# Kernel tuning notes

Measured on AMD Instinct MI355X. Metric: run time of the kernel, lower is better.

## Reference

```python
import jax, jax.numpy as jnp
import numpy as np

OUT = 3      # pooled output size (fmap_size//4 = 14//4 = 3)
RATIO = 2    # roi_align sampling ratio (fixed; torchvision adaptive ratio for 14/3 bins is 2)
P = 20       # num_persons


def _bilinear(fm, y, x):
    # fm: [C,H,W]; y,x broadcastable coordinate grids. torchvision aligned=False semantics.
    C, H, W = fm.shape
    y, x = jnp.broadcast_arrays(y, x)
    valid = (y > -1.0) & (y < H) & (x > -1.0) & (x < W)
    y = jnp.clip(y, 0.0, H - 1.0)
    x = jnp.clip(x, 0.0, W - 1.0)
    y0 = jnp.floor(y).astype(jnp.int32)
    x0 = jnp.floor(x).astype(jnp.int32)
    y1 = jnp.minimum(y0 + 1, H - 1)
    x1 = jnp.minimum(x0 + 1, W - 1)
    ly = y - y0
    lx = x - x0
    hy = 1.0 - ly
    hx = 1.0 - lx
    v00 = fm[:, y0, x0]
    v01 = fm[:, y0, x1]
    v10 = fm[:, y1, x0]
    v11 = fm[:, y1, x1]
    val = hy * hx * v00 + hy * lx * v01 + ly * hx * v10 + ly * lx * v11
    return jnp.where(valid, val, 0.0)  # [C, ...]


def _roi_align_one(fm, box):
    # fm: [C,H,W], box: [4] = (x1,y1,x2,y2) in feature-map coords -> [C,OUT,OUT]
    x1, y1, x2, y2 = box
    bw = (x2 - x1) / OUT
    bh = (y2 - y1) / OUT
    off = (jnp.arange(OUT * RATIO, dtype=fm.dtype) + 0.5) / RATIO  # bin-unit offsets
    xs = x1 + off * bw
    ys = y1 + off * bh
    vals = _bilinear(fm, ys[:, None], xs[None, :])  # [C, OUT*RATIO, OUT*RATIO]
    C = fm.shape[0]
    return vals.reshape(C, OUT, RATIO, OUT, RATIO).mean(axis=(2, 4))


def setup_inputs() -> dict:
    key = jax.random.key(0)
    ks = jax.random.split(key, 8)
    B, N, NB, C, FS = 128, 8, 27, 1024, 14
    fmap = jax.random.normal(ks[0], (B, C, FS, FS), jnp.float32)
    # boxes in feature-map coordinates with x1<x2, y1<y2
    lo = jax.random.uniform(ks[1], (B, N, 2), jnp.float32) * 10.0
    ext = 2.0 + jax.random.uniform(ks[2], (B, N, 2), jnp.float32) * 4.0
    hi = jnp.minimum(lo + ext, float(FS))
    boxes = jnp.concatenate([lo, hi], axis=-1)  # [B,N,4] (x1,y1,x2,y2)
    # unique person ids per frame (scatter target indices)
    pids = jax.vmap(lambda k: jax.random.permutation(k, P)[:N])(jax.random.split(ks[3], B)).astype(jnp.int32)
    w1 = jax.random.normal(ks[4], (512, C), jnp.float32) * 0.02
    w2 = jax.random.normal(ks[5], (256, 512), jnp.float32) * 0.05
    fc1_w = jax.random.normal(ks[6], (1024, 256 * OUT * OUT), jnp.float32) * 0.02
    fc1_b = jnp.zeros((1024,), jnp.float32)
    fc2_w = jax.random.normal(ks[7], (27, 1024), jnp.float32) * 0.02
    fc2_b = jnp.zeros((27,), jnp.float32)
    return {"fmap": fmap, "boxes": boxes, "pids": pids, "w1": w1, "w2": w2,
            "fc1_w": fc1_w, "fc1_b": fc1_b, "fc2_w": fc2_w, "fc2_b": fc2_b}


def _forward(fmap, boxes, pids, w1, w2, fc1_w, fc1_b, fc2_w, fc2_b):
    B, N = boxes.shape[:2]
    # per-image, per-box ROI align: [B,N,C,3,3]
    roi = jax.vmap(jax.vmap(_roi_align_one, in_axes=(None, 0)), in_axes=(0, 0))(fmap, boxes)
    # behavior_conv: two bias-free 1x1 convs (no nonlinearity between)
    h = jnp.einsum('bnchw,oc->bnohw', roi, w1)
    h = jnp.einsum('bnchw,oc->bnohw', h, w2)  # [B,N,256,3,3]
    feat = h.reshape(B, N, -1)                # [B,N,2304]
    bidx = jnp.broadcast_to(jnp.arange(B)[:, None], (B, N))
    # scatter into behavior_tensor keyed by person id (unique pids per frame -> well-defined)
    bt = jnp.zeros((B, P, feat.shape[-1]), feat.dtype).at[bidx, pids].set(feat)
    mean_b = bt.mean(axis=0)                  # [P,2304] mean over batch
    cur = bt[bidx, pids]                      # [B,N,2304]
    diff = mean_b[pids] - cur
    # behavior_fc (dropout is identity at inference)
    h1 = jax.nn.relu(jnp.einsum('bnd,hd->bnh', diff, fc1_w) + fc1_b)
    return jnp.einsum('bnh,oh->bno', h1, fc2_w) + fc2_b  # [B,N,num_behaviors]


def reference(fmap, boxes, pids, w1, w2, fc1_w, fc1_b, fc2_w, fc2_b):
    # fmap is detached and roi_align runs under no_grad in the original
    return _forward(jax.lax.stop_gradient(fmap), jax.lax.stop_gradient(boxes), pids,
                    w1, w2, fc1_w, fc1_b, fc2_w, fc2_b)
```

## Files before the change

### kernel.cpp

```cpp
#include <hip/hip_runtime.h>
#include <hip/hip_bf16.h>
#include <cstddef>
#include <cstdint>

#define B_   128
#define N_   8
#define C_   1024
#define FS_  14
#define POS_ 196
#define P_   20
#define HWC_ 9
#define CMID_ 256
#define FEATD_ 2304
#define H1_  1024
#define O_   27

typedef __attribute__((ext_vector_type(8))) short bf16x8;
typedef __attribute__((ext_vector_type(4))) float f32x4;

__device__ __forceinline__ void gld16(const void* g, void* l) {
    __builtin_amdgcn_global_load_lds(
        (const __attribute__((address_space(1))) unsigned int*)g,
        (__attribute__((address_space(3))) unsigned int*)l, 16, 0, 0);
}

__global__ __launch_bounds__(256) void wcombine_split_kernel(
    const float* __restrict__ w1,
    const float* __restrict__ w2,
    float* __restrict__ wpart)
{
    const int tid = threadIdx.x;
    const int tx = tid & 15, ty = tid >> 4;
    const int c0 = blockIdx.x * 64;
    const int o0 = blockIdx.y * 64;
    const int kb = blockIdx.z * 64;
    __shared__ __align__(16) float As[16][68];
    __shared__ __align__(16) float Bs[16][68];
    float acc[4][4] = {};
    for (int k0 = kb; k0 < kb + 64; k0 += 16) {
        for (int i = tid; i < 64 * 16; i += 256) {
            int k = i & 15, m = i >> 4;
            As[k][m] = w2[(size_t)(o0 + m) * 512 + k0 + k];
        }
        for (int i = tid; i < 64 * 16; i += 256) {
            int n = i & 63, k = i >> 6;
            Bs[k][n] = w1[(size_t)(k0 + k) * 1024 + c0 + n];
        }
        __syncthreads();
        #pragma unroll
        for (int k = 0; k < 16; ++k) {
            float4 a = *(const float4*)&As[k][ty * 4];
            float4 b = *(const float4*)&Bs[k][tx * 4];
            float av[4] = {a.x, a.y, a.z, a.w};
            float bv[4] = {b.x, b.y, b.z, b.w};
            #pragma unroll
            for (int i = 0; i < 4; ++i)
                #pragma unroll
                for (int j = 0; j < 4; ++j)
                    acc[i][j] += av[i] * bv[j];
        }
        __syncthreads();
    }
    float* dst = wpart + (size_t)blockIdx.z * (256 * 1024);
    for (int i = 0; i < 4; ++i) {
        float4 v = make_float4(acc[i][0], acc[i][1], acc[i][2], acc[i][3]);
        *(float4*)&dst[(size_t)(o0 + ty * 4 + i) * 1024 + c0 + tx * 4] = v;
    }
}

__global__ __launch_bounds__(256) void wc_reduce_kernel(
    const float* __restrict__ wpart, __hip_bfloat16* __restrict__ Wc)
{
    int idx = blockIdx.x * 256 + threadIdx.x;
    float s = 0.f;
    #pragma unroll
    for (int z = 0; z < 8; ++z) s += wpart[(size_t)z * (256 * 1024) + idx];
    Wc[idx] = __float2bfloat16(s);
}

#define SSTR_  232
#define AROWS_ 72
#define BOFF_  (AROWS_ * SSTR_)
#define PSTR_  72
#define POFF_  (BOFF_ + 64 * SSTR_)
struct bf4s { __hip_bfloat162 lo, hi; };
__global__ __launch_bounds__(256, 2) void poolmix_kernel(
    const float* __restrict__ fmap,
    const float* __restrict__ boxes,
    const __hip_bfloat16* __restrict__ Wc,
    float* __restrict__ featp)
{
    const int cq = blockIdx.x;
    const int b  = blockIdx.y;
    const int tid = threadIdx.x;
    const int wave = tid >> 6, lane = tid & 63;
    const int m16 = lane & 15, quad = lane >> 4;
    __shared__ __align__(16) __hip_bfloat16 Ls[POFF_ + AROWS_ * PSTR_];

    if (tid < AROWS_) {
        const int m = tid;
        const int n = m / 9, cell = m - n * 9;
        const int chh = cell / 3, cww = cell % 3;
        float4 bx = *(const float4*)(boxes + ((size_t)b * N_ + n) * 4);
        float bw = (bx.z - bx.x) * (1.0f / 3.0f);
        float bh = (bx.w - bx.y) * (1.0f / 3.0f);
        float ypro[FS_], xpro[FS_];
        #pragma unroll
        for (int k = 0; k < FS_; ++k) { ypro[k] = 0.f; xpro[k] = 0.f; }
        #pragma unroll
        for (int s = 0; s < 2; ++s) {
            float yy = bx.y + ((float)(2 * chh + s) + 0.5f) * 0.5f * bh;
            bool vy = (yy > -1.0f) && (yy < (float)FS_);
            float y = fminf(fmaxf(yy, 0.0f), (float)(FS_ - 1));
            int y0 = (int)floorf(y);
            int y1i = min(y0 + 1, FS_ - 1);
            float ly = y - (float)y0, hy = 1.0f - ly;
            float qy = vy ? 0.5f : 0.0f;
            float w0 = hy * qy, w1 = ly * qy;
            #pragma unroll
            for (int k = 0; k < FS_; ++k)
                ypro[k] += (k == y0 ? w0 : 0.f) + (k == y1i ? w1 : 0.f);
            float xx = bx.x + ((float)(2 * cww + s) + 0.5f) * 0.5f * bw;
            bool vx = (xx > -1.0f) && (xx < (float)FS_);
            float x = fminf(fmaxf(xx, 0.0f), (float)(FS_ - 1));
            int x0 = (int)floorf(x);
            int x1i = min(x0 + 1, FS_ - 1);
            float lx = x - (float)x0, hx = 1.0f - lx;
            float qx = vx ? 0.5f : 0.0f;
            float u0 = hx * qx, u1 = lx * qx;
            #pragma unroll
            for (int k = 0; k < FS_; ++k)
                xpro[k] += (k == x0 ? u0 : 0.f) + (k == x1i ? u1 : 0.f);
        }
        __hip_bfloat162* row2 = (__hip_bfloat162*)&Ls[m * SSTR_];
        #pragma unroll
        for (int p = 0; p < 98; ++p) {
            const int i0 = 2 * p, i1 = 2 * p + 1;
            __hip_bfloat162 t;
            t.x = __float2bfloat16(ypro[i0 / FS_] * xpro[i0 % FS_]);
            t.y = __float2bfloat16(ypro[i1 / FS_] * xpro[i1 % FS_]);
            row2[p] = t;
        }
        const __hip_bfloat16 z16 = __float2bfloat16(0.0f);
        #pragma unroll
        for (int p = 98; p < SSTR_ / 2; ++p) {
            __hip_bfloat162 t; t.x = z16; t.y = z16;
            row2[p] = t;
        }
    }
    for (int i = tid; i < 64 * 18; i += 256) {
        int r = i / 18, kd = i - r * 18;
        *(unsigned int*)&Ls[BOFF_ + r * SSTR_ + 196 + kd * 2] = 0;
    }

    f32x4 acc2[5][4];
    #pragma unroll
    for (int mt = 0; mt < 5; ++mt)
        #pragma unroll
        for (int nt = 0; nt < 4; ++nt)
            acc2[mt][nt] = (f32x4){0.f, 0.f, 0.f, 0.f};

    const int cbase0 = cq * 512;
    for (int c = 0; c < 8; ++c) {
        const float* src = fmap + ((size_t)b * C_ + cbase0 + c * 64) * POS_;
        #pragma unroll
        for (int it = 0; it < 13; ++it) {
            int i = tid + it * 256;
            if (i < 64 * 49) {
                int cr = i / 49, ch = i - cr * 49;
                float4 v = *(const float4*)(src + (size_t)cr * POS_ + ch * 4);
                bf4s t;
                t.lo.x = __float2bfloat16(v.x); t.lo.y = __float2bfloat16(v.y);
                t.hi.x = __float2bfloat16(v.z); t.hi.y = __float2bfloat16(v.w);
                *(bf4s*)&Ls[BOFF_ + cr * SSTR_ + ch * 4] = t;
            }
        }
        __syncthreads();

        f32x4 acc1[5];
        #pragma unroll
        for (int mt = 0; mt < 5; ++mt) acc1[mt] = (f32x4){0.f, 0.f, 0.f, 0.f};
        const int nrow = wave * 16 + m16;
        #pragma unroll
        for (int kk = 0; kk < 7; ++kk) {
            bf16x8 bfv = *(const bf16x8*)&Ls[BOFF_ + nrow * SSTR_ + kk * 32 + quad * 8];
            #pragma unroll
            for (int mt = 0; mt < 5; ++mt) {
                bf16x8 af = *(const bf16x8*)&Ls[(mt * 16 + m16) * SSTR_ + kk * 32 + quad * 8];
                acc1[mt] = __builtin_amdgcn_mfma_f32_16x16x32_bf16(af, bfv, acc1[mt], 0, 0, 0);
            }
        }
        #pragma unroll
        for (int mt = 0; mt < 5; ++mt) {
            #pragma unroll
            for (int g = 0; g < 4; ++g) {
                int cell = mt * 16 + quad * 4 + g;
                if (cell < AROWS_)
                    Ls[POFF_ + cell * PSTR_ + wave * 16 + m16] =
                        __float2bfloat16(acc1[mt][g]);
            }
        }
        __syncthreads();

        #pragma unroll
        for (int ks = 0; ks < 2; ++ks) {
            bf16x8 af[5];
            #pragma unroll
            for (int mt = 0; mt < 5; ++mt)
                af[mt] = *(const bf16x8*)&Ls[POFF_ + (mt * 16 + m16) * PSTR_ + ks * 32 + quad * 8];
            #pragma unroll
            for (int nt = 0; nt < 4; ++nt) {
                int n = wave * 64 + nt * 16 + m16;
                bf16x8 bfv = *(const bf16x8*)(Wc + (size_t)n * C_ + cbase0 + c * 64 + ks * 32 + quad * 8);
                #pragma unroll
                for (int mt = 0; mt < 5; ++mt)
                    acc2[mt][nt] = __builtin_amdgcn_mfma_f32_16x16x32_bf16(
                        af[mt], bfv, acc2[mt][nt], 0, 0, 0);
            }
        }
    }

    float* dst = featp + (size_t)cq * (128 * AROWS_ * 256);
    #pragma unroll
    for (int mt = 0; mt < 5; ++mt) {
        #pragma unroll
        for (int g = 0; g < 4; ++g) {
            int row = mt * 16 + quad * 4 + g;
            if (row < AROWS_) {
                #pragma unroll
                for (int nt = 0; nt < 4; ++nt)
                    dst[(size_t)(b * AROWS_ + row) * 256 + wave * 64 + nt * 16 + m16] =
                        acc2[mt][nt][g];
            }
        }
    }
}

__global__ __launch_bounds__(256, 4) void fc1_gemm_kernel(
    const __hip_bfloat16* __restrict__ A,
    const __hip_bfloat16* __restrict__ Bm,
    const float* __restrict__ bias,
    float* __restrict__ C)
{
    const int tid = threadIdx.x;
    const int wave = tid >> 6, lane = tid & 63;
    const int r0 = blockIdx.y * 32, n0 = blockIdx.x * 64;
    const int wm = (wave >> 1) * 16, wn = (wave & 1) * 32;
    const int m16 = lane & 15, quad = lane >> 4;
    const int K = FEATD_;
    __shared__ __align__(16) __hip_bfloat16 As[32 * 64];
    __shared__ __align__(16) __hip_bfloat16 Bs[64 * 64];

    f32x4 acc[2];
    acc[0] = (f32x4){0.f, 0.f, 0.f, 0.f};
    acc[1] = (f32x4){0.f, 0.f, 0.f, 0.f};

    const int qa = wave * 64 + lane;
    const int msA = qa >> 3, csA = (qa & 7) ^ (msA & 7);
    const int qb1 = qa + 256;
    const int msB1 = qb1 >> 3, csB1 = (qb1 & 7) ^ (msB1 & 7);
    const size_t rA  = (size_t)(r0 + msA)  * K + csA  * 8;
    const size_t rB0 = (size_t)(n0 + msA)  * K + csA  * 8;
    const size_t rB1 = (size_t)(n0 + msB1) * K + csB1 * 8;

    for (int k0 = 0; k0 < K; k0 += 64) {
        gld16(A  + rA  + k0, &As[wave * 512]);
        gld16(Bm + rB0 + k0, &Bs[wave * 512]);
        gld16(Bm + rB1 + k0, &Bs[2048 + wave * 512]);
        __syncthreads();
        #pragma unroll
        for (int ks = 0; ks < 2; ++ks) {
            bf16x8 af, bfv[2];
            int m = wm + m16;
            int cp = (ks * 4 + quad) ^ (m & 7);
            af = *(const bf16x8*)&As[(m * 8 + cp) * 8];
            #pragma unroll
            for (int t = 0; t < 2; ++t) {
                int n = wn + t * 16 + m16;
                int cq = (ks * 4 + quad) ^ (n & 7);
                bfv[t] = *(const bf16x8*)&Bs[(n * 8 + cq) * 8];
            }
            #pragma unroll
            for (int j = 0; j < 2; ++j)
                acc[j] = __builtin_amdgcn_mfma_f32_16x16x32_bf16(
                    af, bfv[j], acc[j], 0, 0, 0);
        }
        __syncthreads();
    }

    #pragma unroll
    for (int j = 0; j < 2; ++j) {
        int col = n0 + wn + j * 16 + m16;
        int rbase = r0 + wm + quad * 4;
        float bv = bias[col];
        #pragma unroll
        for (int g = 0; g < 4; ++g) {
            int r = rbase + g;
            float v = acc[j][g] + bv;
            C[(size_t)r * H1_ + col] = v > 0.f ? v : 0.f;
        }
    }
}

__global__ __launch_bounds__(256) void fc1w_perm_kernel(
    const float* __restrict__ src, __hip_bfloat16* __restrict__ dst)
{
    int h = blockIdx.x;
    int tid = threadIdx.x;
    __shared__ float buf[FEATD_];
    const float* s = src + (size_t)h * FEATD_;
    #pragma unroll
    for (int it = 0; it < 9; ++it)
        buf[it * 256 + tid] = s[it * 256 + tid];
    __syncthreads();
    __hip_bfloat16* d = dst + (size_t)h * FEATD_;
    #pragma unroll
    for (int it = 0; it < 9; ++it) {
        int dd = it * 256 + tid;
        d[dd] = __float2bfloat16(buf[tid * HWC_ + it]);
    }
}

__global__ __launch_bounds__(256) void meandiff_kernel(
    const float* __restrict__ fp0, const float* __restrict__ fp1,
    const int* __restrict__ pids, __hip_bfloat16* __restrict__ diff)
{
    int p = blockIdx.x;
    int d = blockIdx.y * 256 + threadIdx.x;
    __shared__ int invs[B_];
    if (threadIdx.x < B_) {
        int bb = threadIdx.x;
        int v = -1;
        #pragma unroll
        for (int n = 0; n < N_; ++n)
            if (pids[bb * N_ + n] == p) v = n;
        invs[bb] = v;
    }
    __syncthreads();

    float acc = 0.0f;
    #pragma unroll 4
    for (int b = 0; b < B_; ++b) {
        int n = invs[b];
        if (n >= 0) {
            size_t idx = (size_t)(b * N_ + n) * FEATD_ + d;
            acc += fp0[idx] + fp1[idx];
        }
    }
    float mean = acc * (1.0f / (float)B_);
    #pragma unroll 4
    for (int b = 0; b < B_; ++b) {
        int n = invs[b];
        if (n >= 0) {
            size_t idx = (size_t)(b * N_ + n) * FEATD_ + d;
            diff[idx] = __float2bfloat16(mean - (fp0[idx] + fp1[idx]));
        }
    }
}

__global__ __launch_bounds__(256) void fc2_kernel(
    const float* __restrict__ h1, const float* __restrict__ fc2_w,
    const float* __restrict__ fc2_b, float* __restrict__ out)
{
    int bn = blockIdx.x;
    int tid = threadIdx.x;
    __shared__ __align__(16) float row[H1_];
    __shared__ float partial[32][8];
    ((float4*)row)[tid] = ((const float4*)(h1 + (size_t)bn * H1_))[tid];
    __syncthreads();
    int o = tid >> 3, part = tid & 7;
    float acc = 0.0f;
    if (o < O_) {
        const float* wrow = fc2_w + (size_t)o * H1_ + part * 128;
        const float* hrow = row + part * 128;
        #pragma unroll 4
        for (int j = 0; j < 128; ++j) acc += hrow[j] * wrow[j];
    }
    partial[o][part] = acc;
    __syncthreads();
    if (part == 0 && o < O_) {
        float s = fc2_b[o];
        #pragma unroll
        for (int p = 0; p < 8; ++p) s += partial[o][p];
        out[(size_t)bn * O_ + o] = s;
    }
}

extern "C" void kernel_launch(void* const* d_in, const int* in_sizes, int n_in,
                              void* d_out, int out_size, void* d_ws, size_t ws_size,
                              hipStream_t stream) {
    const float* fmap  = (const float*)d_in[0];
    const float* boxes = (const float*)d_in[1];
    const int*   pids  = (const int*)  d_in[2];
    const float* w1    = (const float*)d_in[3];
    const float* w2    = (const float*)d_in[4];
    const float* fc1_w = (const float*)d_in[5];
    const float* fc1_b = (const float*)d_in[6];
    const float* fc2_w = (const float*)d_in[7];
    const float* fc2_b = (const float*)d_in[8];
    float* out = (float*)d_out;

    char* wsb = (char*)d_ws;
    __hip_bfloat16* Wc    = (__hip_bfloat16*)wsb;
    __hip_bfloat16* fc1wp = Wc + 256 * 1024;
    __hip_bfloat16* diffp = fc1wp + (size_t)H1_ * FEATD_;
    float* featp  = (float*)(diffp + (size_t)H1_ * FEATD_);
    float* h1     = featp + 2 * (size_t)(B_ * N_) * FEATD_;
    float* wpart  = h1 + (size_t)(B_ * N_) * H1_;
    float* fp0 = featp;
    float* fp1 = featp + (size_t)(B_ * N_) * FEATD_;

    hipLaunchKernelGGL(wcombine_split_kernel, dim3(16, 4, 8), dim3(256), 0, stream,
                       w1, w2, wpart);
    hipLaunchKernelGGL(wc_reduce_kernel, dim3(1024), dim3(256), 0, stream,
                       wpart, Wc);
    hipLaunchKernelGGL(poolmix_kernel, dim3(2, 128), dim3(256), 0, stream,
                       fmap, boxes, Wc, featp);
    hipLaunchKernelGGL(fc1w_perm_kernel, dim3(1024), dim3(256), 0, stream,
                       fc1_w, fc1wp);
    hipLaunchKernelGGL(meandiff_kernel, dim3(20, 9), dim3(256), 0, stream,
                       fp0, fp1, pids, diffp);
    hipLaunchKernelGGL(fc1_gemm_kernel, dim3(16, 32), dim3(256), 0, stream,
                       diffp, fc1wp, fc1_b, h1);
    hipLaunchKernelGGL(fc2_kernel, dim3(1024), dim3(256), 0, stream,
                       h1, fc2_w, fc2_b, out);
}
```

Measured before the change: 297.9 us.

## Split poolmix channels four ways and register-prefetch next fmap chunk

The poolmix kernel now splits the channel dimension into four partitions instead of two, doubling the grid to 4x128 blocks. Each block also prefetches the next 64-channel fmap chunk into registers while the MFMA work on the current chunk runs, then converts and stores it to LDS afterwards. This is meant to hide global load latency and raise parallelism. The costs are twice as many partial-sum buffers for meandiff to read and sum, extra workspace, and 13 float4 registers per thread that may pressure occupancy.

Result: no change. 296.1 us (-0.6%).

```diff
diff --git a/kernel.cpp b/kernel.cpp
--- a/kernel.cpp
+++ b/kernel.cpp
@@ -83,6 +83,7 @@
 #define BOFF_  (AROWS_ * SSTR_)
 #define PSTR_  72
 #define POFF_  (BOFF_ + 64 * SSTR_)
+#define NCHUNK_ 4
 struct bf4s { __hip_bfloat162 lo, hi; };
 __global__ __launch_bounds__(256, 2) void poolmix_kernel(
     const float* __restrict__ fmap,
@@ -152,17 +153,9 @@
         int r = i / 18, kd = i - r * 18;
         *(unsigned int*)&Ls[BOFF_ + r * SSTR_ + 196 + kd * 2] = 0;
     }
-
-    f32x4 acc2[5][4];
-    #pragma unroll
-    for (int mt = 0; mt < 5; ++mt)
-        #pragma unroll
-        for (int nt = 0; nt < 4; ++nt)
-            acc2[mt][nt] = (f32x4){0.f, 0.f, 0.f, 0.f};
-
-    const int cbase0 = cq * 512;
-    for (int c = 0; c < 8; ++c) {
-        const float* src = fmap + ((size_t)b * C_ + cbase0 + c * 64) * POS_;
+    const int cbase0 = cq * 256;
+    {
+        const float* src = fmap + ((size_t)b * C_ + cbase0) * POS_;
         #pragma unroll
         for (int it = 0; it < 13; ++it) {
             int i = tid + it * 256;
@@ -175,7 +168,30 @@
                 *(bf4s*)&Ls[BOFF_ + cr * SSTR_ + ch * 4] = t;
             }
         }
-        __syncthreads();
+    }
+
+    f32x4 acc2[5][4];
+    #pragma unroll
+    for (int mt = 0; mt < 5; ++mt)
+        #pragma unroll
+        for (int nt = 0; nt < 4; ++nt)
+            acc2[mt][nt] = (f32x4){0.f, 0.f, 0.f, 0.f};
+
+    float4 vbuf[13];
+    for (int c = 0; c < NCHUNK_; ++c) {
+        __syncthreads();
+
+        if (c < NCHUNK_ - 1) {
+            const float* src = fmap + ((size_t)b * C_ + cbase0 + (c + 1) * 64) * POS_;
+            #pragma unroll
+            for (int it = 0; it < 13; ++it) {
+                int i = tid + it * 256;
+                if (i < 64 * 49) {
+                    int cr = i / 49, ch = i - cr * 49;
+                    vbuf[it] = *(const float4*)(src + (size_t)cr * POS_ + ch * 4);
+                }
+            }
+        }
 
         f32x4 acc1[5];
         #pragma unroll
@@ -218,9 +234,24 @@
                         af[mt], bfv, acc2[mt][nt], 0, 0, 0);
             }
         }
-    }
-
-    float* dst = featp + (size_t)cq * (128 * AROWS_ * 256);
+
+        if (c < NCHUNK_ - 1) {
+            #pragma unroll
+            for (int it = 0; it < 13; ++it) {
+                int i = tid + it * 256;
+                if (i < 64 * 49) {
+                    int cr = i / 49, ch = i - cr * 49;
+                    float4 v = vbuf[it];
+                    bf4s t;
+                    t.lo.x = __float2bfloat16(v.x); t.lo.y = __float2bfloat16(v.y);
+                    t.hi.x = __float2bfloat16(v.z); t.hi.y = __float2bfloat16(v.w);
+                    *(bf4s*)&Ls[BOFF_ + cr * SSTR_ + ch * 4] = t;
+                }
+            }
+        }
+    }
+
+    float* dst = featp + (size_t)cq * ((size_t)128 * AROWS_ * 256);
     #pragma unroll
     for (int mt = 0; mt < 5; ++mt) {
         #pragma unroll
@@ -322,9 +353,10 @@
 }
 
 __global__ __launch_bounds__(256) void meandiff_kernel(
-    const float* __restrict__ fp0, const float* __restrict__ fp1,
-    const int* __restrict__ pids, __hip_bfloat16* __restrict__ diff)
-{
+    const float* __restrict__ featp, const int* __restrict__ pids,
+    __hip_bfloat16* __restrict__ diff)
+{
+    const size_t PART = (size_t)(B_ * N_) * FEATD_;
     int p = blockIdx.x;
     int d = blockIdx.y * 256 + threadIdx.x;
     __shared__ int invs[B_];
@@ -344,7 +376,8 @@
         int n = invs[b];
         if (n >= 0) {
             size_t idx = (size_t)(b * N_ + n) * FEATD_ + d;
-            acc += fp0[idx] + fp1[idx];
+            acc += (featp[idx] + featp[idx + PART]) +
+                   (featp[idx + 2 * PART] + featp[idx + 3 * PART]);
         }
     }
     float mean = acc * (1.0f / (float)B_);
@@ -353,7 +386,9 @@
         int n = invs[b];
         if (n >= 0) {
             size_t idx = (size_t)(b * N_ + n) * FEATD_ + d;
-            diff[idx] = __float2bfloat16(mean - (fp0[idx] + fp1[idx]));
+            float v = (featp[idx] + featp[idx + PART]) +
+                      (featp[idx + 2 * PART] + featp[idx + 3 * PART]);
+            diff[idx] = __float2bfloat16(mean - v);
         }
     }
 }
@@ -405,21 +440,19 @@
     __hip_bfloat16* fc1wp = Wc + 256 * 1024;
     __hip_bfloat16* diffp = fc1wp + (size_t)H1_ * FEATD_;
     float* featp  = (float*)(diffp + (size_t)H1_ * FEATD_);
-    float* h1     = featp + 2 * (size_t)(B_ * N_) * FEATD_;
+    float* h1     = featp + 4 * (size_t)(B_ * N_) * FEATD_;
     float* wpart  = h1 + (size_t)(B_ * N_) * H1_;
-    float* fp0 = featp;
-    float* fp1 = featp + (size_t)(B_ * N_) * FEATD_;
 
     hipLaunchKernelGGL(wcombine_split_kernel, dim3(16, 4, 8), dim3(256), 0, stream,
                        w1, w2, wpart);
     hipLaunchKernelGGL(wc_reduce_kernel, dim3(1024), dim3(256), 0, stream,
                        wpart, Wc);
-    hipLaunchKernelGGL(poolmix_kernel, dim3(2, 128), dim3(256), 0, stream,
+    hipLaunchKernelGGL(poolmix_kernel, dim3(4, 128), dim3(256), 0, stream,
                        fmap, boxes, Wc, featp);
     hipLaunchKernelGGL(fc1w_perm_kernel, dim3(1024), dim3(256), 0, stream,
                        fc1_w, fc1wp);
     hipLaunchKernelGGL(meandiff_kernel, dim3(20, 9), dim3(256), 0, stream,
-                       fp0, fp1, pids, diffp);
+                       featp, pids, diffp);
     hipLaunchKernelGGL(fc1_gemm_kernel, dim3(16, 32), dim3(256), 0, stream,
                        diffp, fc1wp, fc1_b, h1);
     hipLaunchKernelGGL(fc2_kernel, dim3(1024), dim3(256), 0, stream,
```
